# Performance work log

Hardware: AMD Instinct MI355X
Metric: run time of the kernel (lower is better)

Reference implementation:

```python
import jax, jax.numpy as jnp
import numpy as np

DEPTH, DIM, HEADS, DH, MLP, N, B = 6, 192, 12, 16, 768, 256, 32
INNER = HEADS * DH  # 192


def setup_inputs() -> dict:
    key = jax.random.key(0)
    ks = jax.random.split(key, 10)
    w = lambda i, shape: jax.random.normal(ks[i], shape, dtype=jnp.float32) * 0.02
    return {
        'x': jax.random.normal(ks[0], (B, N, DIM), dtype=jnp.float32),
        'ln1_g': jnp.ones((DEPTH, DIM), jnp.float32),
        'ln1_b': jnp.zeros((DEPTH, DIM), jnp.float32),
        'Wq': w(1, (DEPTH, DIM, INNER)),
        'Wkv': w(2, (DEPTH, DIM, 2 * INNER)),
        'lsa_scale': jnp.full((DEPTH, HEADS), DH ** -0.5, dtype=jnp.float32),
        'mix_pre': jax.random.normal(ks[3], (DEPTH, HEADS, HEADS), dtype=jnp.float32),
        'mix_post': jax.random.normal(ks[4], (DEPTH, HEADS, HEADS), dtype=jnp.float32),
        'Wo': w(5, (DEPTH, INNER, DIM)),
        'bo': jnp.zeros((DEPTH, DIM), jnp.float32),
        'ls1': jnp.full((DEPTH, DIM), 0.1, dtype=jnp.float32),
        'ln2_g': jnp.ones((DEPTH, DIM), jnp.float32),
        'ln2_b': jnp.zeros((DEPTH, DIM), jnp.float32),
        'W1': w(6, (DEPTH, DIM, MLP)),
        'b1': jnp.zeros((DEPTH, MLP), jnp.float32),
        'W2': w(7, (DEPTH, MLP, DIM)),
        'b2': jnp.zeros((DEPTH, DIM), jnp.float32),
        'ls2': jnp.full((DEPTH, DIM), 0.1, dtype=jnp.float32),
    }


def _ln(x, g, b, eps=1e-5):
    m = x.mean(-1, keepdims=True)
    v = ((x - m) ** 2).mean(-1, keepdims=True)
    return (x - m) * jax.lax.rsqrt(v + eps) * g + b


def _heads(t, b, n):
    # (b, n, h*d) -> (b, h, n, d)
    return t.reshape(b, n, HEADS, DH).transpose(0, 2, 1, 3)


def _forward(x, ln1_g, ln1_b, Wq, Wkv, lsa_scale, mix_pre, mix_post, Wo, bo,
             ls1, ln2_g, ln2_b, W1, b1, W2, b2, ls2):
    b, n, _ = x.shape
    diag = jnp.arange(n)
    for l in range(DEPTH):
        # --- PreNorm + talking-heads LSA attention + LayerScale(0.1) ---
        h = _ln(x, ln1_g[l], ln1_b[l])
        q = _heads(h @ Wq[l], b, n)
        k, v = jnp.split(h @ Wkv[l], 2, axis=-1)
        k, v = _heads(k, b, n), _heads(v, b, n)
        dots = jnp.einsum('bhid,bhjd->bhij', q, k) * lsa_scale[l][None, :, None, None]
        # LSA: source sets diagonal to -1e-09 (literal, near-zero) when if_patch_attn
        dots = dots.at[:, :, diag, diag].set(-1e-9)
        dots = jnp.einsum('bhij,hg->bgij', dots, mix_pre[l])
        a = jax.nn.softmax(dots, axis=-1)
        a = jnp.einsum('bhij,hg->bgij', a, mix_post[l])
        o = jnp.einsum('bhij,bhjd->bhid', a, v)
        o = o.transpose(0, 2, 1, 3).reshape(b, n, INNER) @ Wo[l] + bo[l]
        x = x + o * ls1[l]
        # --- PreNorm + GELU FFN + LayerScale(0.1) ---
        h2 = _ln(x, ln2_g[l], ln2_b[l])
        f = jax.nn.gelu(h2 @ W1[l] + b1[l], approximate=False) @ W2[l] + b2[l]
        x = x + f * ls2[l]
    return x


def reference(x, ln1_g, ln1_b, Wq, Wkv, lsa_scale, mix_pre, mix_post, Wo, bo,
              ls1, ln2_g, ln2_b, W1, b1, W2, b2, ls2):
    return _forward(x, ln1_g, ln1_b, Wq, Wkv, lsa_scale, mix_pre, mix_post, Wo,
                    bo, ls1, ln2_g, ln2_b, W1, b1, W2, b2, ls2)
```

## Files before the change

kernel.cpp:

```cpp
#include <hip/hip_runtime.h>
#include <hip/hip_bf16.h>

#define DEPTH   6
#define DIM     192
#define HEADS   12
#define DH      16
#define MLPD    768
#define SEQ     256
#define BATCH   32
#define ROWS    (BATCH*SEQ)

typedef __attribute__((ext_vector_type(8))) short short8;
typedef __attribute__((ext_vector_type(4))) float f32x4;
typedef __attribute__((ext_vector_type(4))) _Float16 half4;
typedef __attribute__((ext_vector_type(8))) _Float16 half8;
typedef __hip_bfloat16 bf16_t;
typedef _Float16 f16_t;

__device__ __forceinline__ bf16_t f2b(float v){ return __float2bfloat16(v); }
__device__ __forceinline__ ushort f2u(float v){
    union{ bf16_t b; ushort u; } w; w.b = __float2bfloat16(v); return w.u;
}
__device__ __forceinline__ f16_t u2h(ushort u){ union{ ushort u; f16_t h; } w; w.u = u; return w.h; }
__device__ __forceinline__ ushort h2u(f16_t h){ union{ ushort u; f16_t h; } w; w.h = h; return w.u; }

__device__ __forceinline__ void async16(ushort* lds, const ushort* gp){
    __builtin_amdgcn_global_load_lds(
        (const __attribute__((address_space(1))) uint*)gp,
        (__attribute__((address_space(3))) uint*)lds, 16, 0, 0);
}

__global__ void copy_kernel(const float* __restrict__ x, float* __restrict__ xr, int n){
    int i = blockIdx.x*256 + threadIdx.x;
    if (i < n) xr[i] = x[i];
}

__device__ __forceinline__ void wt_tile(const float* __restrict__ W,
        ushort* __restrict__ WT, int K, int N, int l, int tx, int ty,
        int tid, ushort* T){
    const float* src = W + ((size_t)l*K + tx*64)*N + ty*64;
    ushort* dst = WT + ((size_t)l*N + ty*64)*K + tx*64;
    int r = tid >> 2, c4 = (tid & 3)*16;
    #pragma unroll
    for (int u=0; u<4; u++){
        float4 v = *(const float4*)(src + (size_t)r*N + c4 + u*4);
        T[(c4+u*4+0)*72 + r] = f2u(v.x);
        T[(c4+u*4+1)*72 + r] = f2u(v.y);
        T[(c4+u*4+2)*72 + r] = f2u(v.z);
        T[(c4+u*4+3)*72 + r] = f2u(v.w);
    }
    __syncthreads();
    int n = tid >> 2, k8 = (tid & 3)*16;
    #pragma unroll
    for (int u=0; u<2; u++)
        *(uint4*)(dst + (size_t)n*K + k8 + u*8) = *(uint4*)&T[n*72 + k8 + u*8];
}

__global__ __launch_bounds__(256) void wt_all(
        const float* __restrict__ Wq, const float* __restrict__ Wkv,
        const float* __restrict__ Wo, const float* __restrict__ W1,
        const float* __restrict__ W2,
        ushort* __restrict__ WqT, ushort* __restrict__ WkvT,
        ushort* __restrict__ WoT, ushort* __restrict__ W1T,
        ushort* __restrict__ W2T){
    __shared__ ushort T[64*72];
    int id = blockIdx.x, l = blockIdx.y, tid = threadIdx.x;
    if (id < 9)       wt_tile(Wq,  WqT,  192, 192, l, id/3,       id%3,       tid, T);
    else if (id < 27) wt_tile(Wkv, WkvT, 192, 384, l, (id-9)/6,   (id-9)%6,   tid, T);
    else if (id < 36) wt_tile(Wo,  WoT,  192, 192, l, (id-27)/3,  (id-27)%3,  tid, T);
    else if (id < 72) wt_tile(W1,  W1T,  192, 768, l, (id-36)/12, (id-36)%12, tid, T);
    else              wt_tile(W2,  W2T,  768, 192, l, (id-72)/3,  (id-72)%3,  tid, T);
}

__global__ __launch_bounds__(256) void ln_kernel(
        const float* __restrict__ xres, const float* __restrict__ ln_g,
        const float* __restrict__ ln_b, ushort* __restrict__ out){
    int lane = threadIdx.x & 63, w = threadIdx.x >> 6;
    int row = blockIdx.x*4 + w;
    const float* xr = xres + (size_t)row*DIM;
    float v0 = xr[lane], v1 = xr[lane+64], v2 = xr[lane+128];
    float s = v0+v1+v2;
    #pragma unroll
    for (int off=32; off; off>>=1) s += __shfl_xor(s, off, 64);
    float m = s*(1.0f/192.0f);
    float d0=v0-m, d1=v1-m, d2=v2-m;
    float q = d0*d0+d1*d1+d2*d2;
    #pragma unroll
    for (int off=32; off; off>>=1) q += __shfl_xor(q, off, 64);
    float inv = rsqrtf(q*(1.0f/192.0f) + 1e-5f);
    float g0 = ln_g[lane], g1 = ln_g[lane+64], g2 = ln_g[lane+128];
    float e0 = ln_b[lane], e1 = ln_b[lane+64], e2 = ln_b[lane+128];
    ushort* dst = out + (size_t)row*DIM;
    dst[lane]     = f2u(d0*inv*g0 + e0);
    dst[lane+64]  = f2u(d1*inv*g1 + e1);
    dst[lane+128] = f2u(d2*inv*g2 + e2);
}

template<int MODE>
__global__ __launch_bounds__(256) void gemm_ln_kernel(
        const ushort* __restrict__ Aln, const ushort* __restrict__ BT0,
        const ushort* __restrict__ BT1, const float* __restrict__ bias,
        f16_t* __restrict__ out0, f16_t* __restrict__ out1,
        f16_t* __restrict__ out2){
    __shared__ ushort As[6*2048];
    __shared__ ushort Bs[6*2048];
    int tid = threadIdx.x, lane = tid & 63, w = tid >> 6;
    int bm = blockIdx.x*64;
    int bn = blockIdx.y*64;
    {
        const ushort* ap = Aln + (size_t)(bm + (tid>>2))*DIM + (tid&3)*8;
        const ushort* bt; int bnl;
        if (MODE == 0 && bn >= DIM){ bt = BT1; bnl = bn - DIM; }
        else { bt = BT0; bnl = bn; }
        const ushort* bp = bt + (size_t)(bnl + (tid>>2))*DIM + (tid&3)*8;
        #pragma unroll
        for (int c=0; c<6; c++){
            async16(&As[c*2048 + tid*8], ap + c*32);
            async16(&Bs[c*2048 + tid*8], bp + c*32);
        }
    }
    __syncthreads();
    int wrow = w >> 1, wcol = w & 1;
    int quad = lane >> 4, mr = lane & 15;
    f32x4 acc[2][2] = {};
    #pragma unroll
    for (int c = 0; c < 6; c++){
        short8 a0 = *(const short8*)&As[c*2048 + (wrow*32+mr)*32    + quad*8];
        short8 a1 = *(const short8*)&As[c*2048 + (wrow*32+16+mr)*32 + quad*8];
        short8 b0 = *(const short8*)&Bs[c*2048 + (wcol*32+mr)*32    + quad*8];
        short8 b1 = *(const short8*)&Bs[c*2048 + (wcol*32+16+mr)*32 + quad*8];
        acc[0][0] = __builtin_amdgcn_mfma_f32_16x16x32_bf16(a0, b0, acc[0][0], 0,0,0);
        acc[0][1] = __builtin_amdgcn_mfma_f32_16x16x32_bf16(a0, b1, acc[0][1], 0,0,0);
        acc[1][0] = __builtin_amdgcn_mfma_f32_16x16x32_bf16(a1, b0, acc[1][0], 0,0,0);
        acc[1][1] = __builtin_amdgcn_mfma_f32_16x16x32_bf16(a1, b1, acc[1][1], 0,0,0);
    }
    #pragma unroll
    for (int rr=0; rr<2; rr++){
        #pragma unroll
        for (int cc=0; cc<2; cc++){
            int col = bn + wcol*32 + cc*16 + mr;
            if (MODE == 0){
                if (col < 2*DIM){
                    f16_t* op = (col < DIM) ? (out0 + col) : (out1 + col - DIM);
                    #pragma unroll
                    for (int tt=0; tt<4; tt++){
                        int row = bm + wrow*32 + rr*16 + quad*4 + tt;
                        op[(size_t)row*DIM] = (f16_t)acc[rr][cc][tt];
                    }
                } else {
                    int d = col - 2*DIM;
                    int row0 = bm + wrow*32 + rr*16 + quad*4;
                    int bb = row0 >> 8, j0 = row0 & 255;
                    half4 pk;
                    #pragma unroll
                    for (int tt=0; tt<4; tt++) pk[tt] = (f16_t)acc[rr][cc][tt];
                    *(half4*)(out2 + (((size_t)(bb*DIM + d)) << 8) + j0) = pk;
                }
            } else {
                float bv = bias[col];
                #pragma unroll
                for (int tt=0; tt<4; tt++){
                    int row = bm + wrow*32 + rr*16 + quad*4 + tt;
                    float z = acc[rr][cc][tt] + bv;
                    ((bf16_t*)out0)[(size_t)row*MLPD + col] =
                        f2b(0.5f*z*(1.0f + erff(z*0.70710678118654752f)));
                }
            }
        }
    }
}

template<int ROUNDS>
__global__ __launch_bounds__(256) void gemm_a_kernel(
        const ushort* __restrict__ A, const ushort* __restrict__ BT,
        const float* __restrict__ bias, const float* __restrict__ ls,
        float* __restrict__ xres){
    const int K = ROUNDS*192;
    __shared__ ushort As[6*2048];
    __shared__ ushort Bs[6*2048];
    int tid = threadIdx.x, lane = tid & 63, w = tid >> 6;
    int wrow = w >> 1, wcol = w & 1;
    int bm = blockIdx.x*64, bn = blockIdx.y*64;
    int quad = lane >> 4, mr = lane & 15;
    const ushort* ap = A  + (size_t)(bm + (tid>>2))*K + (tid&3)*8;
    const ushort* bp = BT + (size_t)(bn + (tid>>2))*K + (tid&3)*8;
    f32x4 acc[2][2] = {};
    for (int r = 0; r < ROUNDS; r++){
        #pragma unroll
        for (int c=0; c<6; c++){
            async16(&As[c*2048 + tid*8], ap + r*192 + c*32);
            async16(&Bs[c*2048 + tid*8], bp + r*192 + c*32);
        }
        __syncthreads();
        #pragma unroll
        for (int c=0; c<6; c++){
            short8 a0 = *(const short8*)&As[c*2048 + (wrow*32+mr)*32    + quad*8];
            short8 a1 = *(const short8*)&As[c*2048 + (wrow*32+16+mr)*32 + quad*8];
            short8 b0 = *(const short8*)&Bs[c*2048 + (wcol*32+mr)*32    + quad*8];
            short8 b1 = *(const short8*)&Bs[c*2048 + (wcol*32+16+mr)*32 + quad*8];
            acc[0][0] = __builtin_amdgcn_mfma_f32_16x16x32_bf16(a0, b0, acc[0][0], 0,0,0);
            acc[0][1] = __builtin_amdgcn_mfma_f32_16x16x32_bf16(a0, b1, acc[0][1], 0,0,0);
            acc[1][0] = __builtin_amdgcn_mfma_f32_16x16x32_bf16(a1, b0, acc[1][0], 0,0,0);
            acc[1][1] = __builtin_amdgcn_mfma_f32_16x16x32_bf16(a1, b1, acc[1][1], 0,0,0);
        }
        if (r+1 < ROUNDS) __syncthreads();
    }
    #pragma unroll
    for (int rr=0; rr<2; rr++){
        #pragma unroll
        for (int cc=0; cc<2; cc++){
            int col = bn + wcol*32 + cc*16 + mr;
            float bv = bias[col], lv = ls[col];
            #pragma unroll
            for (int tt=0; tt<4; tt++){
                int row = bm + wrow*32 + rr*16 + quad*4 + tt;
                xres[(size_t)row*DIM + col] += (acc[rr][cc][tt] + bv)*lv;
            }
        }
    }
}

#define SLAB    4488
#define IST     280
#define KV_OFF  53856
#define VJP     72
#define ROWP    200
#define Q_OFF   67680
#define POST_OFF 70880
#define PRE_OFF 71136
#define LTOT    71280

__global__ __launch_bounds__(1024, 1) void attn_kernel(
        const f16_t* __restrict__ qb, const f16_t* __restrict__ kb,
        const f16_t* __restrict__ vTg,
        const float* __restrict__ lsa, const float* __restrict__ pre,
        const float* __restrict__ post, const ushort* __restrict__ WoT,
        const float* __restrict__ bo, const float* __restrict__ ls1,
        float* __restrict__ xres){
    __shared__ ushort L[LTOT];
    int tid  = threadIdx.x;
    int lane = tid & 63, w = tid >> 6;
    int quad = lane >> 4, nr = lane & 15;
    int b  = blockIdx.x >> 4;
    int i0 = (blockIdx.x & 15) << 4;

    auto stage_v = [&](int c){
        for (int u = tid; u < 1536; u += 1024){
            int e = u*8;
            int d = e >> 6, j = e & 63;
            uint4 v = *(const uint4*)(vTg + (((size_t)(b*DIM + d)) << 8) + c*64 + j);
            *(uint4*)&L[KV_OFF + d*VJP + j] = v;
        }
    };

    if (tid < 384){
        int e = tid*8, i = e/DIM, d = e%DIM, hh = d >> 4;
        float sc = lsa[hh];
        union { uint4 v; f16_t h[8]; } iv, ov;
        iv.v = *(const uint4*)(qb + (size_t)(b*SEQ + i0 + i)*DIM + d);
        #pragma unroll
        for (int u=0; u<8; u++) ov.h[u] = (f16_t)((float)iv.h[u]*sc);
        *(uint4*)&L[Q_OFF + i*ROWP + d] = ov.v;
    } else if (tid < 512){
        for (int k = tid-384; k < 256; k += 128){
            int gg = k >> 4, hh = k & 15;
            L[POST_OFF + k] = (gg < 12 && hh < 12) ? h2u((f16_t)post[hh*12+gg])
                                                   : (ushort)0;
        }
    } else if (tid < 640){
        for (int k = tid-512; k < 144; k += 128)
            L[PRE_OFF + k] = h2u((f16_t)pre[k]);
    }
    stage_v(0);
    __syncthreads();

    half4 postTf = *(const half4*)&L[POST_OFF + nr*16 + quad*4];

    {
        int jg = w*16 + nr;
        const f16_t* krow = kb + (size_t)(b*SEQ + jg)*DIM;
        half8 qh[6], kh[6];
        #pragma unroll
        for (int c=0; c<6; c++){
            union{ short8 s; half8 h; } a, k2;
            a.s  = *(const short8*)&L[Q_OFF + nr*ROWP + c*32 + quad*8];
            k2.s = *(const short8*)(const void*)(krow + c*32 + quad*8);
            qh[c] = a.h; kh[c] = k2.h;
        }
        int dd = jg - (i0 + quad*4);
        int hb = (quad>>1)*12;
        #pragma unroll
        for (int g=0; g<12; g++){
            f32x4 a = {0,0,0,0};
            #pragma unroll
            for (int c=0; c<6; c++){
                f16_t s = u2h(L[PRE_OFF + hb + c*24 + g]);
                a = __builtin_amdgcn_mfma_f32_16x16x32_f16(qh[c]*s, kh[c], a, 0,0,0);
            }
            ushort* sp = &L[g*SLAB + jg];
            sp[(quad*4+0)*IST] = (dd==0) ? (ushort)0 : h2u((f16_t)a[0]);
            sp[(quad*4+1)*IST] = (dd==1) ? (ushort)0 : h2u((f16_t)a[1]);
            sp[(quad*4+2)*IST] = (dd==2) ? (ushort)0 : h2u((f16_t)a[2]);
            sp[(quad*4+3)*IST] = (dd==3) ? (ushort)0 : h2u((f16_t)a[3]);
        }
    }
    __syncthreads();

    for (int r = w; r < 192; r += 16){
        int g = r >> 4, i = r & 15;
        ushort* sp = &L[g*SLAB + i*IST];
        ushort4 uv = *(ushort4*)&sp[lane*4];
        float e0 = __expf((float)u2h(uv.x));
        float e1 = __expf((float)u2h(uv.y));
        float e2 = __expf((float)u2h(uv.z));
        float e3 = __expf((float)u2h(uv.w));
        float ssum = e0+e1+e2+e3;
        #pragma unroll
        for (int off=32; off; off>>=1) ssum += __shfl_xor(ssum, off, 64);
        float rin = 1.0f/ssum;
        uv.x = h2u((f16_t)(e0*rin)); uv.y = h2u((f16_t)(e1*rin));
        uv.z = h2u((f16_t)(e2*rin)); uv.w = h2u((f16_t)(e3*rin));
        *(ushort4*)&sp[lane*4] = uv;
    }
    __syncthreads();

    for (int s = 0; s < 16; s++){
        int cb = s*16 + w;
        int i = cb >> 4, jb = cb & 15;
        int colbase = i*IST + jb*16 + nr;
        half4 bv;
        #pragma unroll
        for (int t=0; t<4; t++){
            int hs = quad*4 + t; if (hs > 11) hs = 11;
            bv[t] = u2h(L[hs*SLAB + colbase]);
        }
        f32x4 cc = __builtin_amdgcn_mfma_f32_16x16x16f16(postTf, bv, (f32x4){0,0,0,0}, 0,0,0);
        if (quad < 3){
            #pragma unroll
            for (int t=0; t<4; t++) L[(quad*4+t)*SLAB + colbase] = h2u((f16_t)cc[t]);
        }
    }
    __syncthreads();

    f32x4 oacc = {0,0,0,0};
    for (int c = 0; c < 4; c++){
        if (w < 12){
            int g = w;
            #pragma unroll
            for (int ks = 0; ks < 4; ks++){
                int jl = ks*16 + quad*4;
                half4 av = *(const half4*)&L[g*SLAB + nr*IST + c*64 + jl];
                half4 bv = *(const half4*)&L[KV_OFF + (g*16 + nr)*VJP + jl];
                oacc = __builtin_amdgcn_mfma_f32_16x16x16f16(av, bv, oacc, 0,0,0);
            }
        }
        if (c < 3){
            __syncthreads();
            stage_v(c+1);
            __syncthreads();
        }
    }

    if (w < 12){
        int g = w;
        #pragma unroll
        for (int t=0; t<4; t++){
            int i = quad*4 + t;
            L[Q_OFF + i*ROWP + g*16 + nr] = f2u(oacc[t]);
        }
    }
    __syncthreads();

    if (w < 12){
        f32x4 wacc = {0,0,0,0};
        int ct = w;
        const ushort* wg = WoT + (size_t)(ct*16 + nr)*192;
        #pragma unroll
        for (int c = 0; c < 3; c++){
            #pragma unroll
            for (int sub = 0; sub < 2; sub++){
                int k0 = c*64 + sub*32;
                short8 av = *(const short8*)&L[Q_OFF + nr*ROWP + k0 + quad*8];
                short8 bv = *(const short8*)(wg + k0 + quad*8);
                wacc = __builtin_amdgcn_mfma_f32_16x16x32_bf16(av, bv, wacc, 0,0,0);
            }
        }
        int col = ct*16 + nr;
        float bv2 = bo[col], lv = ls1[col];
        #pragma unroll
        for (int t=0; t<4; t++){
            int row = b*SEQ + i0 + quad*4 + t;
            xres[(size_t)row*DIM + col] += (wacc[t] + bv2)*lv;
        }
    }
}

extern "C" void kernel_launch(void* const* d_in, const int* in_sizes, int n_in,
                              void* d_out, int out_size, void* d_ws, size_t ws_size,
                              hipStream_t stream){
    const float* x    = (const float*)d_in[0];
    const float* ln1g = (const float*)d_in[1];
    const float* ln1b = (const float*)d_in[2];
    const float* Wq   = (const float*)d_in[3];
    const float* Wkv  = (const float*)d_in[4];
    const float* lsa  = (const float*)d_in[5];
    const float* pre  = (const float*)d_in[6];
    const float* post = (const float*)d_in[7];
    const float* Wo   = (const float*)d_in[8];
    const float* bo   = (const float*)d_in[9];
    const float* ls1  = (const float*)d_in[10];
    const float* ln2g = (const float*)d_in[11];
    const float* ln2b = (const float*)d_in[12];
    const float* W1   = (const float*)d_in[13];
    const float* b1   = (const float*)d_in[14];
    const float* W2   = (const float*)d_in[15];
    const float* b2   = (const float*)d_in[16];
    const float* ls2  = (const float*)d_in[17];
    float* xres = (float*)d_out;

    char* ws = (char*)d_ws;
    f16_t*  qb  = (f16_t*)ws;
    f16_t*  kb  = (f16_t*)(ws + (size_t)ROWS*DIM*2);
    f16_t*  vT  = (f16_t*)(ws + (size_t)ROWS*DIM*4);
    bf16_t* fb  = (bf16_t*)ws;
    char* p = ws + (size_t)ROWS*MLPD*2;
    ushort* WqT  = (ushort*)p; p += (size_t)DEPTH*DIM*DIM*2;
    ushort* WkvT = (ushort*)p; p += (size_t)DEPTH*DIM*2*DIM*2;
    ushort* WoT  = (ushort*)p; p += (size_t)DEPTH*DIM*DIM*2;
    ushort* W1T  = (ushort*)p; p += (size_t)DEPTH*DIM*MLPD*2;
    ushort* W2T  = (ushort*)p; p += (size_t)DEPTH*MLPD*DIM*2;
    ushort* lnb  = (ushort*)p; p += (size_t)ROWS*DIM*2;

    int ntot = ROWS*DIM;
    copy_kernel<<<ntot/256, 256, 0, stream>>>(x, xres, ntot);
    wt_all<<<dim3(108, 6), 256, 0, stream>>>(Wq, Wkv, Wo, W1, W2,
                                             WqT, WkvT, WoT, W1T, W2T);
    for (int l = 0; l < DEPTH; l++){
        ln_kernel<<<ROWS/4, 256, 0, stream>>>(xres, ln1g + l*DIM, ln1b + l*DIM, lnb);
        gemm_ln_kernel<0><<<dim3(128,9), 256, 0, stream>>>(lnb,
                WqT + (size_t)l*DIM*DIM, WkvT + (size_t)l*DIM*2*DIM,
                nullptr, qb, kb, vT);
        attn_kernel<<<BATCH*(SEQ/16), 1024, 0, stream>>>(qb, kb, vT,
                lsa + l*HEADS, pre + l*HEADS*HEADS, post + l*HEADS*HEADS,
                WoT + (size_t)l*DIM*DIM, bo + l*DIM, ls1 + l*DIM, xres);
        ln_kernel<<<ROWS/4, 256, 0, stream>>>(xres, ln2g + l*DIM, ln2b + l*DIM, lnb);
        gemm_ln_kernel<1><<<dim3(128,12), 256, 0, stream>>>(lnb,
                W1T + (size_t)l*DIM*MLPD, nullptr, b1 + l*MLPD, (f16_t*)fb, nullptr,
                nullptr);
        gemm_a_kernel<4><<<dim3(128,3), 256, 0, stream>>>((const ushort*)fb,
                W2T + (size_t)l*MLPD*DIM, b2 + l*DIM, ls2 + l*DIM, xres);
    }
}
```

Measured before the change: 610.5 us.

## Fuse FFN up-projection, GELU and down-projection into one MLP kernel

Replaces the separate W1+GELU GEMM and W2 GEMM with a single kernel. Each block owns 64 rows and loops over 12 chunks of the hidden dimension, keeping GELU outputs in shared memory and accumulating the W2 product in registers. This drops the global write and re-read of the 8192x768 intermediate tensor and one launch per layer. The grid shrinks to only 128 blocks of 512 threads, so fewer CUs may be busy, and the W1/W2 weights are reloaded per block.

```diff
diff --git a/kernel.cpp b/kernel.cpp
--- a/kernel.cpp
+++ b/kernel.cpp
@@ -96,10 +96,9 @@
     dst[lane+128] = f2u(d2*inv*g2 + e2);
 }
 
-template<int MODE>
-__global__ __launch_bounds__(256) void gemm_ln_kernel(
+__global__ __launch_bounds__(256) void gemm_qkv_kernel(
         const ushort* __restrict__ Aln, const ushort* __restrict__ BT0,
-        const ushort* __restrict__ BT1, const float* __restrict__ bias,
+        const ushort* __restrict__ BT1,
         f16_t* __restrict__ out0, f16_t* __restrict__ out1,
         f16_t* __restrict__ out2){
     __shared__ ushort As[6*2048];
@@ -110,7 +109,7 @@
     {
         const ushort* ap = Aln + (size_t)(bm + (tid>>2))*DIM + (tid&3)*8;
         const ushort* bt; int bnl;
-        if (MODE == 0 && bn >= DIM){ bt = BT1; bnl = bn - DIM; }
+        if (bn >= DIM){ bt = BT1; bnl = bn - DIM; }
         else { bt = BT0; bnl = bn; }
         const ushort* bp = bt + (size_t)(bnl + (tid>>2))*DIM + (tid&3)*8;
         #pragma unroll
@@ -139,83 +138,108 @@
         #pragma unroll
         for (int cc=0; cc<2; cc++){
             int col = bn + wcol*32 + cc*16 + mr;
-            if (MODE == 0){
-                if (col < 2*DIM){
-                    f16_t* op = (col < DIM) ? (out0 + col) : (out1 + col - DIM);
-                    #pragma unroll
-                    for (int tt=0; tt<4; tt++){
-                        int row = bm + wrow*32 + rr*16 + quad*4 + tt;
-                        op[(size_t)row*DIM] = (f16_t)acc[rr][cc][tt];
-                    }
-                } else {
-                    int d = col - 2*DIM;
-                    int row0 = bm + wrow*32 + rr*16 + quad*4;
-                    int bb = row0 >> 8, j0 = row0 & 255;
-                    half4 pk;
-                    #pragma unroll
-                    for (int tt=0; tt<4; tt++) pk[tt] = (f16_t)acc[rr][cc][tt];
-                    *(half4*)(out2 + (((size_t)(bb*DIM + d)) << 8) + j0) = pk;
-                }
-            } else {
-                float bv = bias[col];
+            if (col < 2*DIM){
+                f16_t* op = (col < DIM) ? (out0 + col) : (out1 + col - DIM);
                 #pragma unroll
                 for (int tt=0; tt<4; tt++){
                     int row = bm + wrow*32 + rr*16 + quad*4 + tt;
-                    float z = acc[rr][cc][tt] + bv;
-                    ((bf16_t*)out0)[(size_t)row*MLPD + col] =
-                        f2b(0.5f*z*(1.0f + erff(z*0.70710678118654752f)));
+                    op[(size_t)row*DIM] = (f16_t)acc[rr][cc][tt];
                 }
-            }
-        }
-    }
-}
-
-template<int ROUNDS>
-__global__ __launch_bounds__(256) void gemm_a_kernel(
-        const ushort* __restrict__ A, const ushort* __restrict__ BT,
-        const float* __restrict__ bias, const float* __restrict__ ls,
+            } else {
+                int d = col - 2*DIM;
+                int row0 = bm + wrow*32 + rr*16 + quad*4;
+                int bb = row0 >> 8, j0 = row0 & 255;
+                half4 pk;
+                #pragma unroll
+                for (int tt=0; tt<4; tt++) pk[tt] = (f16_t)acc[rr][cc][tt];
+                *(half4*)(out2 + (((size_t)(bb*DIM + d)) << 8) + j0) = pk;
+            }
+        }
+    }
+}
+
+__global__ __launch_bounds__(512, 4) void mlp_kernel(
+        const ushort* __restrict__ Aln, const ushort* __restrict__ W1T,
+        const ushort* __restrict__ W2T, const float* __restrict__ b1,
+        const float* __restrict__ b2, const float* __restrict__ ls2,
         float* __restrict__ xres){
-    const int K = ROUNDS*192;
     __shared__ ushort As[6*2048];
-    __shared__ ushort Bs[6*2048];
+    __shared__ ushort W1s[6*2048];
+    __shared__ ushort W2s[2*6144];
+    __shared__ ushort inter[2*2048];
     int tid = threadIdx.x, lane = tid & 63, w = tid >> 6;
-    int wrow = w >> 1, wcol = w & 1;
-    int bm = blockIdx.x*64, bn = blockIdx.y*64;
     int quad = lane >> 4, mr = lane & 15;
-    const ushort* ap = A  + (size_t)(bm + (tid>>2))*K + (tid&3)*8;
-    const ushort* bp = BT + (size_t)(bn + (tid>>2))*K + (tid&3)*8;
-    f32x4 acc[2][2] = {};
-    for (int r = 0; r < ROUNDS; r++){
+    int bm = blockIdx.x*64;
+
+    #pragma unroll
+    for (int p=0; p<3; p++){
+        int u = p*512 + tid;
+        int c = u >> 8, r = (u >> 2) & 63, k8 = u & 3;
+        async16(&As[u*8],  Aln + (size_t)(bm + r)*DIM + c*32 + k8*8);
+        async16(&W1s[u*8], W1T + (size_t)r*DIM + c*32 + k8*8);
+    }
+    __syncthreads();
+
+    int rt = w >> 1, cg = w & 1;
+    f32x4 acc2[6] = {};
+    for (int m = 0; m < 12; m++){
+        #pragma unroll
+        for (int p=0; p<3; p++){
+            int u = p*512 + tid;
+            int kk = u / 768, rem = u - kk*768;
+            int n = rem >> 2, k8 = rem & 3;
+            async16(&W2s[u*8], W2T + (size_t)n*MLPD + m*64 + kk*32 + k8*8);
+        }
+        f32x4 acc1[2] = {};
         #pragma unroll
         for (int c=0; c<6; c++){
-            async16(&As[c*2048 + tid*8], ap + r*192 + c*32);
-            async16(&Bs[c*2048 + tid*8], bp + r*192 + c*32);
+            short8 av = *(const short8*)&As[c*2048 + (rt*16+mr)*32 + quad*8];
+            #pragma unroll
+            for (int cc=0; cc<2; cc++){
+                short8 bv = *(const short8*)&W1s[c*2048 + (cg*32+cc*16+mr)*32 + quad*8];
+                acc1[cc] = __builtin_amdgcn_mfma_f32_16x16x32_bf16(av, bv, acc1[cc], 0,0,0);
+            }
+        }
+        #pragma unroll
+        for (int cc=0; cc<2; cc++){
+            int col = cg*32 + cc*16 + mr;
+            float bv = b1[m*64 + col];
+            #pragma unroll
+            for (int tt=0; tt<4; tt++){
+                int row = rt*16 + quad*4 + tt;
+                float z = acc1[cc][tt] + bv;
+                inter[(col>>5)*2048 + row*32 + (col&31)] =
+                    f2u(0.5f*z*(1.0f + erff(z*0.70710678118654752f)));
+            }
         }
         __syncthreads();
-        #pragma unroll
-        for (int c=0; c<6; c++){
-            short8 a0 = *(const short8*)&As[c*2048 + (wrow*32+mr)*32    + quad*8];
-            short8 a1 = *(const short8*)&As[c*2048 + (wrow*32+16+mr)*32 + quad*8];
-            short8 b0 = *(const short8*)&Bs[c*2048 + (wcol*32+mr)*32    + quad*8];
-            short8 b1 = *(const short8*)&Bs[c*2048 + (wcol*32+16+mr)*32 + quad*8];
-            acc[0][0] = __builtin_amdgcn_mfma_f32_16x16x32_bf16(a0, b0, acc[0][0], 0,0,0);
-            acc[0][1] = __builtin_amdgcn_mfma_f32_16x16x32_bf16(a0, b1, acc[0][1], 0,0,0);
-            acc[1][0] = __builtin_amdgcn_mfma_f32_16x16x32_bf16(a1, b0, acc[1][0], 0,0,0);
-            acc[1][1] = __builtin_amdgcn_mfma_f32_16x16x32_bf16(a1, b1, acc[1][1], 0,0,0);
-        }
-        if (r+1 < ROUNDS) __syncthreads();
-    }
-    #pragma unroll
-    for (int rr=0; rr<2; rr++){
-        #pragma unroll
-        for (int cc=0; cc<2; cc++){
-            int col = bn + wcol*32 + cc*16 + mr;
-            float bv = bias[col], lv = ls[col];
-            #pragma unroll
-            for (int tt=0; tt<4; tt++){
-                int row = bm + wrow*32 + rr*16 + quad*4 + tt;
-                xres[(size_t)row*DIM + col] += (acc[rr][cc][tt] + bv)*lv;
-            }
+        if (m+1 < 12){
+            #pragma unroll
+            for (int p=0; p<3; p++){
+                int u = p*512 + tid;
+                int c = u >> 8, r = (u >> 2) & 63, k8 = u & 3;
+                async16(&W1s[u*8], W1T + (size_t)((m+1)*64 + r)*DIM + c*32 + k8*8);
+            }
+        }
+        #pragma unroll
+        for (int kk=0; kk<2; kk++){
+            short8 av = *(const short8*)&inter[kk*2048 + (rt*16+mr)*32 + quad*8];
+            #pragma unroll
+            for (int s=0; s<6; s++){
+                short8 bv = *(const short8*)&W2s[kk*6144 + ((cg*6+s)*16+mr)*32 + quad*8];
+                acc2[s] = __builtin_amdgcn_mfma_f32_16x16x32_bf16(av, bv, acc2[s], 0,0,0);
+            }
+        }
+        __syncthreads();
+    }
+    #pragma unroll
+    for (int s=0; s<6; s++){
+        int col = (cg*6+s)*16 + mr;
+        float bv = b2[col], lv = ls2[col];
+        #pragma unroll
+        for (int tt=0; tt<4; tt++){
+            int row = bm + rt*16 + quad*4 + tt;
+            xres[(size_t)row*DIM + col] += (acc2[s][tt] + bv)*lv;
         }
     }
 }
@@ -422,7 +446,6 @@
     f16_t*  qb  = (f16_t*)ws;
     f16_t*  kb  = (f16_t*)(ws + (size_t)ROWS*DIM*2);
     f16_t*  vT  = (f16_t*)(ws + (size_t)ROWS*DIM*4);
-    bf16_t* fb  = (bf16_t*)ws;
     char* p = ws + (size_t)ROWS*MLPD*2;
     ushort* WqT  = (ushort*)p; p += (size_t)DEPTH*DIM*DIM*2;
     ushort* WkvT = (ushort*)p; p += (size_t)DEPTH*DIM*2*DIM*2;
@@ -437,17 +460,15 @@
                                              WqT, WkvT, WoT, W1T, W2T);
     for (int l = 0; l < DEPTH; l++){
         ln_kernel<<<ROWS/4, 256, 0, stream>>>(xres, ln1g + l*DIM, ln1b + l*DIM, lnb);
-        gemm_ln_kernel<0><<<dim3(128,9), 256, 0, stream>>>(lnb,
+        gemm_qkv_kernel<<<dim3(128,9), 256, 0, stream>>>(lnb,
                 WqT + (size_t)l*DIM*DIM, WkvT + (size_t)l*DIM*2*DIM,
-                nullptr, qb, kb, vT);
+                qb, kb, vT);
         attn_kernel<<<BATCH*(SEQ/16), 1024, 0, stream>>>(qb, kb, vT,
                 lsa + l*HEADS, pre + l*HEADS*HEADS, post + l*HEADS*HEADS,
                 WoT + (size_t)l*DIM*DIM, bo + l*DIM, ls1 + l*DIM, xres);
         ln_kernel<<<ROWS/4, 256, 0, stream>>>(xres, ln2g + l*DIM, ln2b + l*DIM, lnb);
-        gemm_ln_kernel<1><<<dim3(128,12), 256, 0, stream>>>(lnb,
-                W1T + (size_t)l*DIM*MLPD, nullptr, b1 + l*MLPD, (f16_t*)fb, nullptr,
-                nullptr);
-        gemm_a_kernel<4><<<dim3(128,3), 256, 0, stream>>>((const ushort*)fb,
-                W2T + (size_t)l*MLPD*DIM, b2 + l*DIM, ls2 + l*DIM, xres);
-    }
-}
+        mlp_kernel<<<128, 512, 0, stream>>>(lnb,
+                W1T + (size_t)l*DIM*MLPD, W2T + (size_t)l*MLPD*DIM,
+                b1 + l*MLPD, b2 + l*DIM, ls2 + l*DIM, xres);
+    }
+}
```

Measured after the change: 663.7 us. 8.7% more time.
